# Kernel optimization log

Measured on AMD Instinct MI355X. Metric: run time of the kernel, lower is better.

## Reference

```python
import jax, jax.numpy as jnp
import numpy as np

EMBED_DIM = 1024
NUM_HEADS = 32
MULT = 2                      # edit_channel_multiply_factor
HPM = NUM_HEADS // MULT       # heads_per_multiply = 16
HEAD_DIM = EMBED_DIM * MULT // NUM_HEADS  # 64


def setup_inputs() -> dict:
    key = jax.random.key(0)
    ks = jax.random.split(key, 8)
    B, Q, S, D = 8, 4096, 128, EMBED_DIM
    return {
        "encoder_hidden_states": jax.random.normal(ks[0], (B, Q, D), dtype=jnp.float32),
        "hidden_states": jax.random.normal(ks[1], (B, S, D), dtype=jnp.float32),
        # Conv1D weights are [nx, nf] (input-major, like GPT-2), std=0.02; biases zero
        "q_w": jax.random.normal(ks[2], (MULT, D, D), dtype=jnp.float32) * 0.02,
        "q_b": jnp.zeros((MULT, D), dtype=jnp.float32),
        "c_attn_w": jax.random.normal(ks[3], (MULT, D, 2 * D), dtype=jnp.float32) * 0.02,
        "c_attn_b": jnp.zeros((MULT, 2 * D), dtype=jnp.float32),
        "c_proj_w": jax.random.normal(ks[4], (MULT, D, D), dtype=jnp.float32) * 0.02,
        "c_proj_b": jnp.zeros((MULT, D), dtype=jnp.float32),
    }


def _forward(encoder_hidden_states, hidden_states, q_w, q_b,
             c_attn_w, c_attn_b, c_proj_w, c_proj_b):
    B, Q, D = encoder_hidden_states.shape
    # last-token hidden state supplies K/V (kv_len == 1)
    h_last = hidden_states[:, -1, :]                                  # [B, D]

    # all M projections batched via einsum over the multiply dim 'm'
    q = jnp.einsum("bqe,mef->mbqf", encoder_hidden_states, q_w) \
        + q_b[:, None, None, :]                                       # [M, B, Q, D]
    kv = jnp.einsum("be,mef->mbf", h_last, c_attn_w) \
        + c_attn_b[:, None, :]                                        # [M, B, 2D]
    k, v = kv[..., :D], kv[..., D:]                                   # [M, B, D]

    # split heads: D = HPM * HEAD_DIM
    q = q.reshape(MULT, B, Q, HPM, HEAD_DIM)                          # [M,B,Q,H,d]
    k = k.reshape(MULT, B, HPM, HEAD_DIM)                             # [M,B,H,d]
    v = v.reshape(MULT, B, HPM, HEAD_DIM)

    # GPT2 eager attention with a single key: scores [M,B,H,Q] (kv=1)
    scores = jnp.einsum("mbqhd,mbhd->mbhq", q, k) / jnp.sqrt(
        jnp.asarray(HEAD_DIM, dtype=q.dtype))
    # softmax over the kv axis (size 1) -> identically 1, kept for fidelity
    w = jax.nn.softmax(scores[..., None], axis=-1)                    # [M,B,H,Q,1]
    attn = w * v[:, :, :, None, :]                                    # [M,B,H,Q,d]

    # merge heads -> [M, B, Q, D], then output projection
    attn = attn.transpose(0, 1, 3, 2, 4).reshape(MULT, B, Q, D)
    out_m = jnp.einsum("mbqd,mde->mbqe", attn, c_proj_w) \
        + c_proj_b[:, None, None, :]                                  # [M,B,Q,D]

    # faithful accumulation: outputs[0][0] += attn_output[0] for i > 0
    # (only batch element 0 receives contributions from multiplies > 0)
    out = out_m[0]
    out = out.at[0].add(jnp.sum(out_m[1:, 0], axis=0))
    return out


def reference(encoder_hidden_states, hidden_states, q_w, q_b,
              c_attn_w, c_attn_b, c_proj_w, c_proj_b):
    return _forward(encoder_hidden_states, hidden_states, q_w, q_b,
                    c_attn_w, c_attn_b, c_proj_w, c_proj_b)
```

## Files before the change

### kernel.cpp

```cpp
#include <hip/hip_runtime.h>

#define DIM    1024
#define BATCH  8
#define QLEN   4096
#define SEQ    128
#define NMULT  2

typedef float vfloat4 __attribute__((ext_vector_type(4)));

__global__ void __launch_bounds__(256) kernelA(const float* __restrict__ hidden,
                                               const float* __restrict__ c_attn_w,
                                               float* __restrict__ vp) {
    __shared__ float h_s[BATCH][64];
    __shared__ vfloat4 vred[16][16][9];

    const int tid = threadIdx.x;
    const int es = blockIdx.x & 15;
    const int c  = (blockIdx.x >> 4) & 15;
    const int m  = blockIdx.x >> 8;

    if (tid < 128) {
        int b = tid >> 4, e4 = tid & 15;
        const vfloat4* src = reinterpret_cast<const vfloat4*>(
            hidden + (size_t)b * (SEQ * DIM) + (size_t)(SEQ - 1) * DIM + es * 64);
        reinterpret_cast<vfloat4*>(h_s[b])[e4] = src[e4];
    }
    __syncthreads();

    const int d4 = tid & 15;
    const int eg = tid >> 4;
    const float* wbase = c_attn_w + (size_t)m * DIM * (2 * DIM) + DIM + c * 64 + d4 * 4;

    vfloat4 acc[BATCH];
#pragma unroll
    for (int b = 0; b < BATCH; ++b) acc[b] = (vfloat4){0.f, 0.f, 0.f, 0.f};

#pragma unroll
    for (int k = 0; k < 4; ++k) {
        int el = eg * 4 + k;
        int e  = es * 64 + el;
        vfloat4 w4 = *reinterpret_cast<const vfloat4*>(wbase + (size_t)e * (2 * DIM));
#pragma unroll
        for (int b = 0; b < BATCH; ++b) acc[b] += h_s[b][el] * w4;
    }
#pragma unroll
    for (int b = 0; b < BATCH; ++b) vred[eg][d4][b] = acc[b];
    __syncthreads();

    if (tid < 128) {
        int b = tid >> 4, dq = tid & 15;
        vfloat4 s = vred[0][dq][b];
#pragma unroll
        for (int g = 1; g < 16; ++g) s += vred[g][dq][b];
        reinterpret_cast<vfloat4*>(vp)[es * 4096 + (m * BATCH + b) * 256 + c * 16 + dq] = s;
    }
}

__global__ void __launch_bounds__(256) kernelB(const float* __restrict__ vp,
                                               const float* __restrict__ c_attn_b,
                                               const float* __restrict__ c_proj_w,
                                               float* __restrict__ yp) {
    __shared__ float v_s[BATCH][64];
    __shared__ vfloat4 yred[16][16][9];

    const int tid = threadIdx.x;
    const int ce = blockIdx.x & 15;
    const int cd = (blockIdx.x >> 4) & 15;
    const int m  = blockIdx.x >> 8;

    if (tid < 128) {
        int b = tid >> 4, d4 = tid & 15;
        vfloat4 s = reinterpret_cast<const vfloat4*>(
            c_attn_b + (size_t)m * 2 * DIM + DIM)[cd * 16 + d4];
        const vfloat4* vp4 = reinterpret_cast<const vfloat4*>(vp);
#pragma unroll
        for (int es = 0; es < 16; ++es) {
            s += vp4[es * 4096 + (m * BATCH + b) * 256 + cd * 16 + d4];
        }
        reinterpret_cast<vfloat4*>(v_s[b])[d4] = s;
    }
    __syncthreads();

    const int e4 = tid & 15;
    const int dg = tid >> 4;
    const float* wbase = c_proj_w + (size_t)m * DIM * DIM + ce * 64 + e4 * 4;

    vfloat4 acc[BATCH];
#pragma unroll
    for (int b = 0; b < BATCH; ++b) acc[b] = (vfloat4){0.f, 0.f, 0.f, 0.f};

#pragma unroll
    for (int j = 0; j < 4; ++j) {
        int dl = dg * 4 + j;
        int d  = cd * 64 + dl;
        vfloat4 w4 = *reinterpret_cast<const vfloat4*>(wbase + (size_t)d * DIM);
#pragma unroll
        for (int b = 0; b < BATCH; ++b) acc[b] += v_s[b][dl] * w4;
    }
#pragma unroll
    for (int b = 0; b < BATCH; ++b) yred[dg][e4][b] = acc[b];
    __syncthreads();

    if (tid < 128) {
        int b = tid >> 4, eq = tid & 15;
        vfloat4 s = yred[0][eq][b];
#pragma unroll
        for (int g = 1; g < 16; ++g) s += yred[g][eq][b];
        reinterpret_cast<vfloat4*>(yp)[cd * 4096 + (m * BATCH + b) * 256 + ce * 16 + eq] = s;
    }
}

__global__ void __launch_bounds__(256) bcast_reduce(const float* __restrict__ yp,
                                                    const float* __restrict__ c_proj_b,
                                                    float* __restrict__ out) {
    int b = blockIdx.x >> 8;
    int q0 = (blockIdx.x & 255) * 16;
    int t = threadIdx.x;

    const vfloat4* bias4 = reinterpret_cast<const vfloat4*>(c_proj_b);
    const vfloat4* yp4 = reinterpret_cast<const vfloat4*>(yp);
    vfloat4 val = bias4[t];
#pragma unroll
    for (int cd = 0; cd < 16; ++cd) {
        val += yp4[cd * 4096 + b * 256 + t];
    }
    if (b == 0) {
        val += bias4[256 + t];
#pragma unroll
        for (int cd = 0; cd < 16; ++cd) {
            val += yp4[cd * 4096 + BATCH * 256 + t];
        }
    }

    vfloat4* o = reinterpret_cast<vfloat4*>(out) + ((size_t)b * QLEN + q0) * 256 + t;
#pragma unroll
    for (int q = 0; q < 16; ++q) {
        __builtin_nontemporal_store(val, o + (size_t)q * 256);
    }
}

extern "C" void kernel_launch(void* const* d_in, const int* in_sizes, int n_in,
                              void* d_out, int out_size, void* d_ws, size_t ws_size,
                              hipStream_t stream) {
    const float* hidden   = (const float*)d_in[1];
    const float* c_attn_w = (const float*)d_in[4];
    const float* c_attn_b = (const float*)d_in[5];
    const float* c_proj_w = (const float*)d_in[6];
    const float* c_proj_b = (const float*)d_in[7];
    float* out = (float*)d_out;

    float* vp = (float*)d_ws;
    float* yp = vp + 16 * 16384;

    kernelA<<<512, 256, 0, stream>>>(hidden, c_attn_w, vp);
    kernelB<<<512, 256, 0, stream>>>(vp, c_attn_b, c_proj_w, yp);
    bcast_reduce<<<2048, 256, 0, stream>>>(yp, c_proj_b, out);
}
```

Baseline: 37.96 us.

## Double split-K grid for GEMV kernels and reduce kernelB partials via atomics

Halves the reduction slice per block in both GEMV kernels, doubling the grid to 1024 blocks. kernelB now accumulates its partial products directly into a bias-initialised output vector with float atomicAdd, instead of writing 16 partial slabs for the broadcast kernel to sum. The broadcast kernel then reads one vector per batch. This trades more parallelism and a smaller final reduction for atomic contention and non-deterministic summation order.

```diff
diff --git a/kernel.cpp b/kernel.cpp
--- a/kernel.cpp
+++ b/kernel.cpp
@@ -10,19 +10,26 @@
 
 __global__ void __launch_bounds__(256) kernelA(const float* __restrict__ hidden,
                                                const float* __restrict__ c_attn_w,
-                                               float* __restrict__ vp) {
-    __shared__ float h_s[BATCH][64];
+                                               const float* __restrict__ c_proj_b,
+                                               float* __restrict__ vp,
+                                               float* __restrict__ y) {
+    __shared__ float h_s[BATCH][32];
     __shared__ vfloat4 vred[16][16][9];
 
     const int tid = threadIdx.x;
-    const int es = blockIdx.x & 15;
-    const int c  = (blockIdx.x >> 4) & 15;
-    const int m  = blockIdx.x >> 8;
+    const int es = blockIdx.x & 31;
+    const int c  = (blockIdx.x >> 5) & 15;
+    const int m  = blockIdx.x >> 9;
 
-    if (tid < 128) {
-        int b = tid >> 4, e4 = tid & 15;
+    if (c == 0 && es < BATCH) {
+        reinterpret_cast<vfloat4*>(y)[(m * BATCH + es) * 256 + tid] =
+            reinterpret_cast<const vfloat4*>(c_proj_b)[m * 256 + tid];
+    }
+
+    if (tid < 64) {
+        int b = tid >> 3, e4 = tid & 7;
         const vfloat4* src = reinterpret_cast<const vfloat4*>(
-            hidden + (size_t)b * (SEQ * DIM) + (size_t)(SEQ - 1) * DIM + es * 64);
+            hidden + (size_t)b * (SEQ * DIM) + (size_t)(SEQ - 1) * DIM + es * 32);
         reinterpret_cast<vfloat4*>(h_s[b])[e4] = src[e4];
     }
     __syncthreads();
@@ -36,9 +43,9 @@
     for (int b = 0; b < BATCH; ++b) acc[b] = (vfloat4){0.f, 0.f, 0.f, 0.f};
 
 #pragma unroll
-    for (int k = 0; k < 4; ++k) {
-        int el = eg * 4 + k;
-        int e  = es * 64 + el;
+    for (int k = 0; k < 2; ++k) {
+        int el = eg * 2 + k;
+        int e  = es * 32 + el;
         vfloat4 w4 = *reinterpret_cast<const vfloat4*>(wbase + (size_t)e * (2 * DIM));
 #pragma unroll
         for (int b = 0; b < BATCH; ++b) acc[b] += h_s[b][el] * w4;
@@ -59,23 +66,23 @@
 __global__ void __launch_bounds__(256) kernelB(const float* __restrict__ vp,
                                                const float* __restrict__ c_attn_b,
                                                const float* __restrict__ c_proj_w,
-                                               float* __restrict__ yp) {
-    __shared__ float v_s[BATCH][64];
+                                               float* __restrict__ y) {
+    __shared__ float v_s[BATCH][32];
     __shared__ vfloat4 yred[16][16][9];
 
     const int tid = threadIdx.x;
     const int ce = blockIdx.x & 15;
-    const int cd = (blockIdx.x >> 4) & 15;
-    const int m  = blockIdx.x >> 8;
+    const int cd = (blockIdx.x >> 4) & 31;
+    const int m  = blockIdx.x >> 9;
 
-    if (tid < 128) {
-        int b = tid >> 4, d4 = tid & 15;
+    if (tid < 64) {
+        int b = tid >> 3, d4 = tid & 7;
         vfloat4 s = reinterpret_cast<const vfloat4*>(
-            c_attn_b + (size_t)m * 2 * DIM + DIM)[cd * 16 + d4];
+            c_attn_b + (size_t)m * 2 * DIM + DIM)[cd * 8 + d4];
         const vfloat4* vp4 = reinterpret_cast<const vfloat4*>(vp);
 #pragma unroll
-        for (int es = 0; es < 16; ++es) {
-            s += vp4[es * 4096 + (m * BATCH + b) * 256 + cd * 16 + d4];
+        for (int es = 0; es < 32; ++es) {
+            s += vp4[es * 4096 + (m * BATCH + b) * 256 + cd * 8 + d4];
         }
         reinterpret_cast<vfloat4*>(v_s[b])[d4] = s;
     }
@@ -90,9 +97,9 @@
     for (int b = 0; b < BATCH; ++b) acc[b] = (vfloat4){0.f, 0.f, 0.f, 0.f};
 
 #pragma unroll
-    for (int j = 0; j < 4; ++j) {
-        int dl = dg * 4 + j;
-        int d  = cd * 64 + dl;
+    for (int j = 0; j < 2; ++j) {
+        int dl = dg * 2 + j;
+        int d  = cd * 32 + dl;
         vfloat4 w4 = *reinterpret_cast<const vfloat4*>(wbase + (size_t)d * DIM);
 #pragma unroll
         for (int b = 0; b < BATCH; ++b) acc[b] += v_s[b][dl] * w4;
@@ -106,30 +113,24 @@
         vfloat4 s = yred[0][eq][b];
 #pragma unroll
         for (int g = 1; g < 16; ++g) s += yred[g][eq][b];
-        reinterpret_cast<vfloat4*>(yp)[cd * 4096 + (m * BATCH + b) * 256 + ce * 16 + eq] = s;
+        float* dst = y + (size_t)(m * BATCH + b) * DIM + ce * 64 + eq * 4;
+        atomicAdd(dst + 0, s.x);
+        atomicAdd(dst + 1, s.y);
+        atomicAdd(dst + 2, s.z);
+        atomicAdd(dst + 3, s.w);
     }
 }
 
-__global__ void __launch_bounds__(256) bcast_reduce(const float* __restrict__ yp,
-                                                    const float* __restrict__ c_proj_b,
+__global__ void __launch_bounds__(256) bcast_kernel(const float* __restrict__ y,
                                                     float* __restrict__ out) {
     int b = blockIdx.x >> 8;
     int q0 = (blockIdx.x & 255) * 16;
     int t = threadIdx.x;
 
-    const vfloat4* bias4 = reinterpret_cast<const vfloat4*>(c_proj_b);
-    const vfloat4* yp4 = reinterpret_cast<const vfloat4*>(yp);
-    vfloat4 val = bias4[t];
-#pragma unroll
-    for (int cd = 0; cd < 16; ++cd) {
-        val += yp4[cd * 4096 + b * 256 + t];
-    }
+    const vfloat4* y4 = reinterpret_cast<const vfloat4*>(y);
+    vfloat4 val = y4[b * 256 + t];
     if (b == 0) {
-        val += bias4[256 + t];
-#pragma unroll
-        for (int cd = 0; cd < 16; ++cd) {
-            val += yp4[cd * 4096 + BATCH * 256 + t];
-        }
+        val += y4[BATCH * 256 + t];
     }
 
     vfloat4* o = reinterpret_cast<vfloat4*>(out) + ((size_t)b * QLEN + q0) * 256 + t;
@@ -150,9 +151,9 @@
     float* out = (float*)d_out;
 
     float* vp = (float*)d_ws;
-    float* yp = vp + 16 * 16384;
+    float* y  = vp + 32 * 16384;
 
-    kernelA<<<512, 256, 0, stream>>>(hidden, c_attn_w, vp);
-    kernelB<<<512, 256, 0, stream>>>(vp, c_attn_b, c_proj_w, yp);
-    bcast_reduce<<<2048, 256, 0, stream>>>(yp, c_proj_b, out);
+    kernelA<<<1024, 256, 0, stream>>>(hidden, c_attn_w, c_proj_b, vp, y);
+    kernelB<<<1024, 256, 0, stream>>>(vp, c_attn_b, c_proj_w, y);
+    bcast_kernel<<<2048, 256, 0, stream>>>(y, out);
 }
```

New measurement: 48.52 us. 27.8% more time.

## Fuse V projection and output projection into one kernel with redundant V compute

Applied to the files above, without the earlier changes.

Merges the V-projection and c_proj kernels into one launch. Each block recomputes its 64-wide slice of v over the full input dimension instead of reading split-K partial sums from the workspace. This removes a kernel launch and the intermediate partial-sum buffer, at the cost of 16x redundant V-weight reads and longer serial work per block.

```diff
diff --git a/kernel.cpp b/kernel.cpp
--- a/kernel.cpp
+++ b/kernel.cpp
@@ -4,108 +4,94 @@
 #define BATCH  8
 #define QLEN   4096
 #define SEQ    128
-#define NMULT  2
 
 typedef float vfloat4 __attribute__((ext_vector_type(4)));
 
-__global__ void __launch_bounds__(256) kernelA(const float* __restrict__ hidden,
-                                               const float* __restrict__ c_attn_w,
-                                               float* __restrict__ vp) {
-    __shared__ float h_s[BATCH][64];
-    __shared__ vfloat4 vred[16][16][9];
-
-    const int tid = threadIdx.x;
-    const int es = blockIdx.x & 15;
-    const int c  = (blockIdx.x >> 4) & 15;
-    const int m  = blockIdx.x >> 8;
-
-    if (tid < 128) {
-        int b = tid >> 4, e4 = tid & 15;
-        const vfloat4* src = reinterpret_cast<const vfloat4*>(
-            hidden + (size_t)b * (SEQ * DIM) + (size_t)(SEQ - 1) * DIM + es * 64);
-        reinterpret_cast<vfloat4*>(h_s[b])[e4] = src[e4];
-    }
-    __syncthreads();
-
-    const int d4 = tid & 15;
-    const int eg = tid >> 4;
-    const float* wbase = c_attn_w + (size_t)m * DIM * (2 * DIM) + DIM + c * 64 + d4 * 4;
-
-    vfloat4 acc[BATCH];
-#pragma unroll
-    for (int b = 0; b < BATCH; ++b) acc[b] = (vfloat4){0.f, 0.f, 0.f, 0.f};
-
-#pragma unroll
-    for (int k = 0; k < 4; ++k) {
-        int el = eg * 4 + k;
-        int e  = es * 64 + el;
-        vfloat4 w4 = *reinterpret_cast<const vfloat4*>(wbase + (size_t)e * (2 * DIM));
-#pragma unroll
-        for (int b = 0; b < BATCH; ++b) acc[b] += h_s[b][el] * w4;
-    }
-#pragma unroll
-    for (int b = 0; b < BATCH; ++b) vred[eg][d4][b] = acc[b];
-    __syncthreads();
-
-    if (tid < 128) {
-        int b = tid >> 4, dq = tid & 15;
-        vfloat4 s = vred[0][dq][b];
-#pragma unroll
-        for (int g = 1; g < 16; ++g) s += vred[g][dq][b];
-        reinterpret_cast<vfloat4*>(vp)[es * 4096 + (m * BATCH + b) * 256 + c * 16 + dq] = s;
-    }
-}
-
-__global__ void __launch_bounds__(256) kernelB(const float* __restrict__ vp,
-                                               const float* __restrict__ c_attn_b,
-                                               const float* __restrict__ c_proj_w,
-                                               float* __restrict__ yp) {
+__global__ void __launch_bounds__(256) fused_vy(const float* __restrict__ hidden,
+                                                const float* __restrict__ c_attn_w,
+                                                const float* __restrict__ c_attn_b,
+                                                const float* __restrict__ c_proj_w,
+                                                float* __restrict__ yp) {
+    __shared__ float h_ch[BATCH][256];
+    __shared__ vfloat4 red[16][16][9];
     __shared__ float v_s[BATCH][64];
-    __shared__ vfloat4 yred[16][16][9];
 
     const int tid = threadIdx.x;
     const int ce = blockIdx.x & 15;
     const int cd = (blockIdx.x >> 4) & 15;
     const int m  = blockIdx.x >> 8;
 
+    const int d4 = tid & 15;
+    const int eg = tid >> 4;
+
+    const float* wv = c_attn_w + (size_t)m * DIM * (2 * DIM) + DIM + cd * 64 + d4 * 4;
+    vfloat4 acc[BATCH];
+#pragma unroll
+    for (int b = 0; b < BATCH; ++b) acc[b] = (vfloat4){0.f, 0.f, 0.f, 0.f};
+
+    for (int ch = 0; ch < 4; ++ch) {
+#pragma unroll
+        for (int k = 0; k < 2; ++k) {
+            int idx = tid + 256 * k;
+            int hb = idx >> 6;
+            int c4 = idx & 63;
+            reinterpret_cast<vfloat4*>(h_ch[hb])[c4] =
+                reinterpret_cast<const vfloat4*>(
+                    hidden + (size_t)hb * (SEQ * DIM) + (size_t)(SEQ - 1) * DIM
+                    + ch * 256)[c4];
+        }
+        __syncthreads();
+#pragma unroll
+        for (int j = 0; j < 16; ++j) {
+            int el = eg * 16 + j;
+            int e  = ch * 256 + el;
+            vfloat4 w4 = *reinterpret_cast<const vfloat4*>(wv + (size_t)e * (2 * DIM));
+#pragma unroll
+            for (int b = 0; b < BATCH; ++b) acc[b] += h_ch[b][el] * w4;
+        }
+        __syncthreads();
+    }
+
+#pragma unroll
+    for (int b = 0; b < BATCH; ++b) red[eg][d4][b] = acc[b];
+    __syncthreads();
+
     if (tid < 128) {
-        int b = tid >> 4, d4 = tid & 15;
-        vfloat4 s = reinterpret_cast<const vfloat4*>(
-            c_attn_b + (size_t)m * 2 * DIM + DIM)[cd * 16 + d4];
-        const vfloat4* vp4 = reinterpret_cast<const vfloat4*>(vp);
+        int b = tid >> 4, dq = tid & 15;
+        vfloat4 s = red[0][dq][b];
 #pragma unroll
-        for (int es = 0; es < 16; ++es) {
-            s += vp4[es * 4096 + (m * BATCH + b) * 256 + cd * 16 + d4];
-        }
-        reinterpret_cast<vfloat4*>(v_s[b])[d4] = s;
+        for (int g = 1; g < 16; ++g) s += red[g][dq][b];
+        vfloat4 bias = *reinterpret_cast<const vfloat4*>(
+            c_attn_b + (size_t)m * 2 * DIM + DIM + cd * 64 + dq * 4);
+        reinterpret_cast<vfloat4*>(v_s[b])[dq] = s + bias;
     }
     __syncthreads();
 
     const int e4 = tid & 15;
     const int dg = tid >> 4;
-    const float* wbase = c_proj_w + (size_t)m * DIM * DIM + ce * 64 + e4 * 4;
+    const float* wp = c_proj_w + (size_t)m * DIM * DIM + ce * 64 + e4 * 4;
 
-    vfloat4 acc[BATCH];
+    vfloat4 acc2[BATCH];
 #pragma unroll
-    for (int b = 0; b < BATCH; ++b) acc[b] = (vfloat4){0.f, 0.f, 0.f, 0.f};
+    for (int b = 0; b < BATCH; ++b) acc2[b] = (vfloat4){0.f, 0.f, 0.f, 0.f};
 
 #pragma unroll
     for (int j = 0; j < 4; ++j) {
         int dl = dg * 4 + j;
         int d  = cd * 64 + dl;
-        vfloat4 w4 = *reinterpret_cast<const vfloat4*>(wbase + (size_t)d * DIM);
+        vfloat4 w4 = *reinterpret_cast<const vfloat4*>(wp + (size_t)d * DIM);
 #pragma unroll
-        for (int b = 0; b < BATCH; ++b) acc[b] += v_s[b][dl] * w4;
+        for (int b = 0; b < BATCH; ++b) acc2[b] += v_s[b][dl] * w4;
     }
 #pragma unroll
-    for (int b = 0; b < BATCH; ++b) yred[dg][e4][b] = acc[b];
+    for (int b = 0; b < BATCH; ++b) red[dg][e4][b] = acc2[b];
     __syncthreads();
 
     if (tid < 128) {
         int b = tid >> 4, eq = tid & 15;
-        vfloat4 s = yred[0][eq][b];
+        vfloat4 s = red[0][eq][b];
 #pragma unroll
-        for (int g = 1; g < 16; ++g) s += yred[g][eq][b];
+        for (int g = 1; g < 16; ++g) s += red[g][eq][b];
         reinterpret_cast<vfloat4*>(yp)[cd * 4096 + (m * BATCH + b) * 256 + ce * 16 + eq] = s;
     }
 }
@@ -149,10 +135,8 @@
     const float* c_proj_b = (const float*)d_in[7];
     float* out = (float*)d_out;
 
-    float* vp = (float*)d_ws;
-    float* yp = vp + 16 * 16384;
+    float* yp = (float*)d_ws;
 
-    kernelA<<<512, 256, 0, stream>>>(hidden, c_attn_w, vp);
-    kernelB<<<512, 256, 0, stream>>>(vp, c_attn_b, c_proj_w, yp);
+    fused_vy<<<512, 256, 0, stream>>>(hidden, c_attn_w, c_attn_b, c_proj_w, yp);
     bcast_reduce<<<2048, 256, 0, stream>>>(yp, c_proj_b, out);
 }
```

Result: slower. 43.80 us (+15.4%).

## Repartition output projection per batch to drop split-K partials and reduction pass

Applied to the files above, without the earlier changes.

kernelB now gives each block one (m, b, 32-column) slice and has it reduce over the full 1024-long input dimension itself, with a shared-memory tree reduction, so it writes final y values with bias folded in. The broadcast kernel then only loads one vector per batch instead of summing 16 partial slices. The cost is that each block re-reads its 1024x32 weight slab once per batch element, so c_proj_w traffic rises roughly eightfold (mostly served from L2), and the tree reduction adds several barriers.

```diff
diff --git a/kernel.cpp b/kernel.cpp
--- a/kernel.cpp
+++ b/kernel.cpp
@@ -4,7 +4,6 @@
 #define BATCH  8
 #define QLEN   4096
 #define SEQ    128
-#define NMULT  2
 
 typedef float vfloat4 __attribute__((ext_vector_type(4)));
 
@@ -59,77 +58,63 @@
 __global__ void __launch_bounds__(256) kernelB(const float* __restrict__ vp,
                                                const float* __restrict__ c_attn_b,
                                                const float* __restrict__ c_proj_w,
-                                               float* __restrict__ yp) {
-    __shared__ float v_s[BATCH][64];
-    __shared__ vfloat4 yred[16][16][9];
+                                               const float* __restrict__ c_proj_b,
+                                               float* __restrict__ y) {
+    __shared__ float v_s[DIM];
+    __shared__ vfloat4 red[32][9];
 
     const int tid = threadIdx.x;
-    const int ce = blockIdx.x & 15;
-    const int cd = (blockIdx.x >> 4) & 15;
+    const int ce = blockIdx.x & 31;
+    const int b  = (blockIdx.x >> 5) & 7;
     const int m  = blockIdx.x >> 8;
 
-    if (tid < 128) {
-        int b = tid >> 4, d4 = tid & 15;
+    {
         vfloat4 s = reinterpret_cast<const vfloat4*>(
-            c_attn_b + (size_t)m * 2 * DIM + DIM)[cd * 16 + d4];
+            c_attn_b + (size_t)m * 2 * DIM + DIM)[tid];
         const vfloat4* vp4 = reinterpret_cast<const vfloat4*>(vp);
 #pragma unroll
         for (int es = 0; es < 16; ++es) {
-            s += vp4[es * 4096 + (m * BATCH + b) * 256 + cd * 16 + d4];
+            s += vp4[es * 4096 + (m * BATCH + b) * 256 + tid];
         }
-        reinterpret_cast<vfloat4*>(v_s[b])[d4] = s;
+        reinterpret_cast<vfloat4*>(v_s)[tid] = s;
     }
     __syncthreads();
 
-    const int e4 = tid & 15;
-    const int dg = tid >> 4;
-    const float* wbase = c_proj_w + (size_t)m * DIM * DIM + ce * 64 + e4 * 4;
+    const int e4 = tid & 7;
+    const int dg = tid >> 3;
+    const float* wp = c_proj_w + (size_t)m * DIM * DIM + ce * 32 + e4 * 4;
 
-    vfloat4 acc[BATCH];
+    vfloat4 acc = {0.f, 0.f, 0.f, 0.f};
+#pragma unroll 8
+    for (int j = 0; j < 32; ++j) {
+        int d = dg + 32 * j;
+        vfloat4 w4 = *reinterpret_cast<const vfloat4*>(wp + (size_t)d * DIM);
+        acc += v_s[d] * w4;
+    }
+    red[dg][e4] = acc;
+    __syncthreads();
 #pragma unroll
-    for (int b = 0; b < BATCH; ++b) acc[b] = (vfloat4){0.f, 0.f, 0.f, 0.f};
-
-#pragma unroll
-    for (int j = 0; j < 4; ++j) {
-        int dl = dg * 4 + j;
-        int d  = cd * 64 + dl;
-        vfloat4 w4 = *reinterpret_cast<const vfloat4*>(wbase + (size_t)d * DIM);
-#pragma unroll
-        for (int b = 0; b < BATCH; ++b) acc[b] += v_s[b][dl] * w4;
+    for (int s = 16; s >= 1; s >>= 1) {
+        if (dg < s) red[dg][e4] += red[dg + s][e4];
+        __syncthreads();
     }
-#pragma unroll
-    for (int b = 0; b < BATCH; ++b) yred[dg][e4][b] = acc[b];
-    __syncthreads();
-
-    if (tid < 128) {
-        int b = tid >> 4, eq = tid & 15;
-        vfloat4 s = yred[0][eq][b];
-#pragma unroll
-        for (int g = 1; g < 16; ++g) s += yred[g][eq][b];
-        reinterpret_cast<vfloat4*>(yp)[cd * 4096 + (m * BATCH + b) * 256 + ce * 16 + eq] = s;
+    if (tid < 8) {
+        vfloat4 bias = reinterpret_cast<const vfloat4*>(c_proj_b)[m * 256 + ce * 8 + tid];
+        reinterpret_cast<vfloat4*>(y)[(m * BATCH + b) * 256 + ce * 8 + tid] =
+            red[0][tid] + bias;
     }
 }
 
-__global__ void __launch_bounds__(256) bcast_reduce(const float* __restrict__ yp,
-                                                    const float* __restrict__ c_proj_b,
+__global__ void __launch_bounds__(256) bcast_kernel(const float* __restrict__ y,
                                                     float* __restrict__ out) {
     int b = blockIdx.x >> 8;
     int q0 = (blockIdx.x & 255) * 16;
     int t = threadIdx.x;
 
-    const vfloat4* bias4 = reinterpret_cast<const vfloat4*>(c_proj_b);
-    const vfloat4* yp4 = reinterpret_cast<const vfloat4*>(yp);
-    vfloat4 val = bias4[t];
-#pragma unroll
-    for (int cd = 0; cd < 16; ++cd) {
-        val += yp4[cd * 4096 + b * 256 + t];
-    }
+    const vfloat4* y4 = reinterpret_cast<const vfloat4*>(y);
+    vfloat4 val = y4[b * 256 + t];
     if (b == 0) {
-        val += bias4[256 + t];
-#pragma unroll
-        for (int cd = 0; cd < 16; ++cd) {
-            val += yp4[cd * 4096 + BATCH * 256 + t];
-        }
+        val += y4[BATCH * 256 + t];
     }
 
     vfloat4* o = reinterpret_cast<vfloat4*>(out) + ((size_t)b * QLEN + q0) * 256 + t;
@@ -150,9 +135,9 @@
     float* out = (float*)d_out;
 
     float* vp = (float*)d_ws;
-    float* yp = vp + 16 * 16384;
+    float* y  = vp + 16 * 16384;
 
     kernelA<<<512, 256, 0, stream>>>(hidden, c_attn_w, vp);
-    kernelB<<<512, 256, 0, stream>>>(vp, c_attn_b, c_proj_w, yp);
-    bcast_reduce<<<2048, 256, 0, stream>>>(yp, c_proj_b, out);
+    kernelB<<<512, 256, 0, stream>>>(vp, c_attn_b, c_proj_w, c_proj_b, y);
+    bcast_kernel<<<2048, 256, 0, stream>>>(y, out);
 }
```

New measurement: 41.32 us. +8.9%, slower.
